# Optimization experiments

Hardware: AMD Instinct MI355X
Metric: run time of the kernel (lower is better)

## Reference

```python
import jax, jax.numpy as jnp
import numpy as np

N_NODES = 50000
N_EDGES = 800000
FEAT = 128
HID = 128
NUM_GRAPHS = 64
ODE_STEPS = 8   # fixed-step RK4 stand-in for adaptive odeint over CFG.ode_time_points
DEPTH = 1.0
EPS = 1e-5


def layer_norm(x, g, b):
    m = jnp.mean(x, axis=-1, keepdims=True)
    v = jnp.var(x, axis=-1, keepdims=True)
    return (x - m) * jax.lax.rsqrt(v + EPS) * g + b


def setup_inputs() -> dict:
    key = jax.random.key(0)
    ks = jax.random.split(key, 16)
    s = 1.0 / np.sqrt(FEAT)
    sh = 1.0 / np.sqrt(HID)
    inp = {
        "x": jax.random.normal(ks[0], (N_NODES, FEAT), jnp.float32),
        "edge_index": jax.random.randint(ks[1], (2, N_EDGES), 0, N_NODES, jnp.int64),
        "batch": jnp.sort(jax.random.randint(ks[2], (N_NODES,), 0, NUM_GRAPHS, jnp.int64)),
        "alpha": jnp.float32(0.8),
        "beta": jnp.float32(0.6),
        "phase": jnp.float32(0.7),
        "W_in": jax.random.normal(ks[3], (FEAT, HID), jnp.float32) * s,
        "b_in": jnp.zeros((HID,), jnp.float32),
        "g_in": jnp.ones((HID,), jnp.float32),
        "be_in": jnp.zeros((HID,), jnp.float32),
        "W_alt": jax.random.normal(ks[4], (FEAT, HID), jnp.float32) * s,
        "b_alt": jnp.zeros((HID,), jnp.float32),
        "g_alt": jnp.ones((HID,), jnp.float32),
        "be_alt": jnp.zeros((HID,), jnp.float32),
        "W_self": jax.random.normal(ks[5], (HID, HID), jnp.float32) * sh,
        "W_msg": jax.random.normal(ks[6], (HID, HID), jnp.float32) * sh,
        "b_ode": jnp.zeros((HID,), jnp.float32),
        "W_int": jax.random.normal(ks[7], (2 * HID, HID), jnp.float32) * sh / np.sqrt(2.0),
        "b_int": jnp.zeros((HID,), jnp.float32),
        "g_int": jnp.ones((HID,), jnp.float32),
        "be_int": jnp.zeros((HID,), jnp.float32),
        "W_out": jax.random.normal(ks[8], (HID, HID), jnp.float32) * sh,
        "b_out": jnp.zeros((HID,), jnp.float32),
    }
    return inp


def _forward(x, alpha, beta, phase,
             W_in, b_in, g_in, be_in,
             W_alt, b_alt, g_alt, be_alt,
             W_self, W_msg, b_ode,
             W_int, b_int, g_int, be_int,
             W_out, b_out,
             edge_index, batch):
    src, dst = edge_index[0], edge_index[1]
    # in-degree for mean aggregation (clamped to 1)
    deg = jax.ops.segment_sum(jnp.ones((src.shape[0],), jnp.float32), dst,
                              num_segments=N_NODES)
    deg = jnp.maximum(deg, 1.0)[:, None]

    # quantum amplitudes -> measurement probabilities (normalized)
    norm = jnp.sqrt(alpha ** 2 + beta ** 2)
    a, b = alpha / norm, beta / norm
    p0, p1 = a ** 2, b ** 2

    # two projection pathways in superposition
    h0 = jax.nn.gelu(layer_norm(x @ W_in + b_in, g_in, be_in))
    h1 = jax.nn.gelu(layer_norm(x @ W_alt + b_alt, g_alt, be_alt))
    h = jnp.sqrt(p0) * h0 + jnp.sqrt(p1) * h1  # [N, H]

    # Neural ODE: dh/dt = tanh(h W_self + mean_{j->i}(h_j W_msg) + b)
    def ode_f(h):
        msg = h[src] @ W_msg                       # [E, H] gather + GEMM
        agg = jax.ops.segment_sum(msg, dst, num_segments=N_NODES) / deg
        return jnp.tanh(h @ W_self + agg + b_ode)

    dt = jnp.float32(DEPTH / ODE_STEPS)

    def rk4_step(h, _):
        k1 = ode_f(h)
        k2 = ode_f(h + 0.5 * dt * k1)
        k3 = ode_f(h + 0.5 * dt * k2)
        k4 = ode_f(h + dt * k3)
        return h + (dt / 6.0) * (k1 + 2.0 * k2 + 2.0 * k3 + k4), None

    h, _ = jax.lax.scan(rk4_step, h, None, length=ODE_STEPS)

    # quantum interference mixing (conditional branch -> masked add)
    interf = 2.0 * jnp.sqrt(p0 * p1) * jnp.cos(phase)
    h_int = jnp.tanh(layer_norm(jnp.concatenate([h, h], axis=-1) @ W_int + b_int,
                                g_int, be_int))
    gate = jnp.where(jnp.abs(interf) > 0.01, interf, 0.0)
    h = h + gate * h_int

    # eval-mode collapse: if p1 >= p0, scale by Re(e^{i*phase}) = cos(phase)
    h = jnp.where(p0 > p1, h, h * jnp.cos(phase))

    h_out = h @ W_out + b_out

    # global mean pool over graphs
    cnt = jax.ops.segment_sum(jnp.ones((N_NODES,), jnp.float32), batch,
                              num_segments=NUM_GRAPHS)
    pooled = jax.ops.segment_sum(h_out, batch, num_segments=NUM_GRAPHS)
    return pooled / jnp.maximum(cnt, 1.0)[:, None]  # [NUM_GRAPHS, H]


def reference(x, edge_index, batch, alpha, beta, phase,
              W_in, b_in, g_in, be_in,
              W_alt, b_alt, g_alt, be_alt,
              W_self, W_msg, b_ode,
              W_int, b_int, g_int, be_int,
              W_out, b_out):
    return _forward(x, alpha, beta, phase,
                    W_in, b_in, g_in, be_in,
                    W_alt, b_alt, g_alt, be_alt,
                    W_self, W_msg, b_ode,
                    W_int, b_int, g_int, be_int,
                    W_out, b_out, edge_index, batch)
```

## Files before the change

### kernel.cpp

```cpp
#include <hip/hip_runtime.h>
#include <math.h>

#define NND 50000
#define NED 800000
#define HD  128
#define NG  64
#define MT  64

typedef __attribute__((ext_vector_type(8))) short short8v;
typedef __attribute__((ext_vector_type(4))) float float4v;
typedef __attribute__((ext_vector_type(2))) float float2v;

__device__ __forceinline__ float gelu_t(float x) {
  const float c = 0.7978845608028654f;
  float t = tanhf(c * (x + 0.044715f * x * x * x));
  return 0.5f * x * (1.0f + t);
}

__device__ __forceinline__ unsigned short f2bf(float f) {
  unsigned int u = __float_as_uint(f);
  u += 0x7FFFu + ((u >> 16) & 1u);
  return (unsigned short)(u >> 16);
}
__device__ __forceinline__ float bf2f(unsigned short s) {
  return __uint_as_float(((unsigned int)s) << 16);
}
__device__ __forceinline__ float bflo(unsigned int u) { return __uint_as_float(u << 16); }
__device__ __forceinline__ float bfhi(unsigned int u) { return __uint_as_float(u & 0xFFFF0000u); }
__device__ __forceinline__ unsigned char f2fp8(float f) {
  return (unsigned char)(__builtin_amdgcn_cvt_pk_fp8_f32(f, f, 0, false) & 0xFF);
}

__global__ void k_hist(const int* __restrict__ dst, int* __restrict__ degi) {
  int e = blockIdx.x * 256 + threadIdx.x;
  if (e < NED) atomicAdd(&degi[dst[e]], 1);
}

__global__ __launch_bounds__(1024) void k_scan(
    const int* __restrict__ degi, int* __restrict__ rowptr,
    int* __restrict__ cursor, float* __restrict__ deginv) {
  __shared__ int wsum[16];
  int tid = threadIdx.x;
  int lane = tid & 63;
  int wid = tid >> 6;
  int running = 0;
  for (int base = 0; base < NND; base += 1024) {
    int idx = base + tid;
    int v = (idx < NND) ? degi[idx] : 0;
    int s = v;
#pragma unroll
    for (int o = 1; o < 64; o <<= 1) {
      int t = __shfl_up(s, o, 64);
      if (lane >= o) s += t;
    }
    if (lane == 63) wsum[wid] = s;
    __syncthreads();
    if (wid == 0) {
      int ws = (lane < 16) ? wsum[lane] : 0;
#pragma unroll
      for (int o = 1; o < 16; o <<= 1) {
        int t = __shfl_up(ws, o, 64);
        if (lane >= o) ws += t;
      }
      if (lane < 16) wsum[lane] = ws;
    }
    __syncthreads();
    int woff = wid ? wsum[wid - 1] : 0;
    int excl = running + woff + s - v;
    if (idx < NND) {
      rowptr[idx] = excl;
      cursor[idx] = excl;
      deginv[idx] = 1.0f / (float)max(v, 1);
    }
    int tot = wsum[15];
    __syncthreads();
    running += tot;
  }
  if (tid == 0) rowptr[NND] = running;
}

__global__ void k_scatter(const int* __restrict__ src, const int* __restrict__ dst,
                          int* __restrict__ cursor, int* __restrict__ csrsrc) {
  int e = blockIdx.x * 256 + threadIdx.x;
  if (e < NED) {
    int d = dst[e];
    int pos = atomicAdd(&cursor[d], 1);
    csrsrc[pos] = src[e];
  }
}

__global__ void k_cnt(const int* __restrict__ batch, float* __restrict__ cnt) {
  int g = threadIdx.x;
  if (g >= NG) return;
  int lo, hi, ub_g, ub_gm1;
  lo = 0; hi = NND;
  while (lo < hi) { int mid = (lo + hi) >> 1; if (batch[mid] <= g) lo = mid + 1; else hi = mid; }
  ub_g = lo;
  if (g == 0) ub_gm1 = 0;
  else {
    lo = 0; hi = NND;
    int v = g - 1;
    while (lo < hi) { int mid = (lo + hi) >> 1; if (batch[mid] <= v) lo = mid + 1; else hi = mid; }
    ub_gm1 = lo;
  }
  cnt[g] = (float)(ub_g - ub_gm1);
}

__global__ void k_weff(const float* __restrict__ Wint, float* __restrict__ weff) {
  int i = blockIdx.x * 256 + threadIdx.x;
  if (i < HD * HD) weff[i] = Wint[i] + Wint[i + HD * HD];
}

__global__ void k_prepB(const float* __restrict__ Wself, const float* __restrict__ Wmsg,
                        unsigned short* __restrict__ Bt) {
  int i = blockIdx.x * 256 + threadIdx.x;
  if (i < 128 * 256) {
    int n = i >> 8, k = i & 255;
    float w = (k < HD) ? Wself[k * HD + n] : Wmsg[(k - HD) * HD + n];
    Bt[i] = f2bf(w);
  }
}

__global__ void k_prepIn(const float* __restrict__ Win, const float* __restrict__ Walt,
                         unsigned short* __restrict__ BtIn) {
  int i = blockIdx.x * 256 + threadIdx.x;
  if (i < 2 * 128 * 128) {
    int p = i >> 14; int rem = i & 16383; int n = rem >> 7; int k = rem & 127;
    const float* W = p ? Walt : Win;
    BtIn[i] = f2bf(W[k * 128 + n]);
  }
}

__global__ __launch_bounds__(256) void k_init2(
    const float* __restrict__ x, const unsigned short* __restrict__ BtIn,
    const float* __restrict__ bin, const float* __restrict__ gin, const float* __restrict__ bein,
    const float* __restrict__ balt, const float* __restrict__ galt, const float* __restrict__ bealt,
    const float* __restrict__ alphap, const float* __restrict__ betap,
    float* __restrict__ hdst, unsigned short* __restrict__ hbf)
{
  __shared__ float red[4][16][2];
  __shared__ unsigned short gtile[2][16][64];
  int tid = threadIdx.x;
  int wave = tid >> 6;
  int lane = tid & 63;
  int l15 = lane & 15;
  int lhi = lane >> 4;
  int path = wave >> 1;
  int colBase = (wave & 1) * 64;
  int rowBase = blockIdx.x * 64;

  const unsigned short* Bp = BtIn + path * 128 * 128;
  short8v bfr[4][4];
#pragma unroll
  for (int t = 0; t < 4; ++t) {
    int n = colBase + t * 16 + l15;
#pragma unroll
    for (int s = 0; s < 4; ++s)
      bfr[t][s] = *(const short8v*)&Bp[n * 128 + s * 32 + lhi * 8];
  }

  const float* bvp = path ? balt : bin;
  const float* gp  = path ? galt : gin;
  const float* bep = path ? bealt : bein;
  float bv[4], gw[4], bew[4];
#pragma unroll
  for (int t = 0; t < 4; ++t) {
    int col = colBase + t * 16 + l15;
    bv[t] = bvp[col]; gw[t] = gp[col]; bew[t] = bep[col];
  }

  float al = alphap[0], btv = betap[0];
  float nrm = sqrtf(al * al + btv * btv);
  float w0 = fabsf(al) / nrm, w1 = fabsf(btv) / nrm;

  for (int rt = 0; rt < 4; ++rt) {
    int arow = rowBase + rt * 16 + l15; if (arow >= NND) arow = NND - 1;
    short8v afr[4];
#pragma unroll
    for (int s = 0; s < 4; ++s) {
      float4 xa = *(const float4*)&x[(size_t)arow * HD + s * 32 + lhi * 8];
      float4 xb = *(const float4*)&x[(size_t)arow * HD + s * 32 + lhi * 8 + 4];
      short8v f;
      f[0] = (short)f2bf(xa.x); f[1] = (short)f2bf(xa.y);
      f[2] = (short)f2bf(xa.z); f[3] = (short)f2bf(xa.w);
      f[4] = (short)f2bf(xb.x); f[5] = (short)f2bf(xb.y);
      f[6] = (short)f2bf(xb.z); f[7] = (short)f2bf(xb.w);
      afr[s] = f;
    }

    float4v acc[4];
#pragma unroll
    for (int t = 0; t < 4; ++t) acc[t] = (float4v){0.f, 0.f, 0.f, 0.f};
#pragma unroll
    for (int s = 0; s < 4; ++s) {
#pragma unroll
      for (int t = 0; t < 4; ++t)
        acc[t] = __builtin_amdgcn_mfma_f32_16x16x32_bf16(afr[s], bfr[t][s], acc[t], 0, 0, 0);
    }

    float z[4][4];
    float psum[4], psq[4];
#pragma unroll
    for (int r = 0; r < 4; ++r) {
      float s1 = 0.f, s2 = 0.f;
#pragma unroll
      for (int t = 0; t < 4; ++t) {
        float zz = acc[t][r] + bv[t];
        z[r][t] = zz;
        s1 += zz; s2 += zz * zz;
      }
#pragma unroll
      for (int m = 1; m < 16; m <<= 1) {
        s1 += __shfl_xor(s1, m, 16);
        s2 += __shfl_xor(s2, m, 16);
      }
      psum[r] = s1; psq[r] = s2;
    }
    if (l15 == 0) {
#pragma unroll
      for (int r = 0; r < 4; ++r) {
        red[wave][lhi * 4 + r][0] = psum[r];
        red[wave][lhi * 4 + r][1] = psq[r];
      }
    }
    __syncthreads();

    int pw = wave ^ 1;
    float gval[4][4];
#pragma unroll
    for (int r = 0; r < 4; ++r) {
      int rowl = lhi * 4 + r;
      float S = psum[r] + red[pw][rowl][0];
      float Q = psq[r]  + red[pw][rowl][1];
      float mean = S * (1.0f / 128.0f);
      float var  = Q * (1.0f / 128.0f) - mean * mean;
      float rs = rsqrtf(var + 1e-5f);
#pragma unroll
      for (int t = 0; t < 4; ++t)
        gval[r][t] = gelu_t((z[r][t] - mean) * rs * gw[t] + bew[t]);
    }

    if (path == 1) {
#pragma unroll
      for (int r = 0; r < 4; ++r)
#pragma unroll
        for (int t = 0; t < 4; ++t)
          gtile[wave & 1][lhi * 4 + r][t * 16 + l15] = f2bf(gval[r][t]);
    }
    __syncthreads();

    if (path == 0) {
#pragma unroll
      for (int r = 0; r < 4; ++r) {
        int m = rowBase + rt * 16 + lhi * 4 + r;
        if (m < NND) {
#pragma unroll
          for (int t = 0; t < 4; ++t) {
            float g1 = bf2f(gtile[wave & 1][lhi * 4 + r][t * 16 + l15]);
            float hv = w0 * gval[r][t] + w1 * g1;
            size_t off = (size_t)m * HD + colBase + t * 16 + l15;
            hdst[off] = hv;
            hbf[off] = f2bf(hv);
          }
        }
      }
    }
    __syncthreads();
  }
}

__global__ __launch_bounds__(256) void k_fused(
    const unsigned short* __restrict__ ain,
    const unsigned short* __restrict__ hbf,
    const unsigned char* __restrict__ k8r,
    unsigned char* __restrict__ k8w,
    unsigned short* __restrict__ usav,
    const int* __restrict__ rowptr, const int* __restrict__ csrsrc,
    const float* __restrict__ deginv,
    const unsigned short* __restrict__ Bt, const float* __restrict__ bode,
    const float* __restrict__ h, float* __restrict__ hacc,
    float* __restrict__ hout, unsigned short* __restrict__ ybf,
    unsigned short* __restrict__ hbfout, int stage)
{
  __shared__ unsigned char u_lds[MT * 256];
  int tid = threadIdx.x;
  int wave = tid >> 6;
  int lane = tid & 63;
  int l15 = lane & 15;
  int lhi = lane >> 4;
  int rowBase = blockIdx.x * MT;
  int ncol0 = wave * 32;

  const float DT = 0.125f;
  float wk = (stage == 0 || stage == 3) ? DT / 6.0f : DT / 3.0f;
  float cy = (stage <= 1) ? 0.5f * DT : DT;
  float cu = (stage == 3) ? DT : 0.5f * DT;

  if (stage == 0) {
    int l16 = tid & 15;
    int grp = tid >> 4;
#pragma unroll
    for (int g = 0; g < MT / 16; ++g) {
      int nloc = g * 16 + grp;
      int node = rowBase + nloc;
      if (node < NND) {
        int e0 = rowptr[node], e1 = rowptr[node + 1];
        float a0=0,a1=0,a2=0,a3=0,a4=0,a5=0,a6=0,a7=0;
        for (int eb = e0; eb < e1; eb += 8) {
          int n8 = e1 - eb; if (n8 > 8) n8 = 8;
          int sidx[8];
#pragma unroll
          for (int j = 0; j < 8; ++j) sidx[j] = csrsrc[eb + ((j < n8) ? j : 0)];
#pragma unroll
          for (int j = 0; j < 8; ++j) {
            if (j < n8) {
              uint4 v = *(const uint4*)&hbf[(size_t)sidx[j] * HD + l16 * 8];
              a0 += bflo(v.x); a1 += bfhi(v.x); a2 += bflo(v.y); a3 += bfhi(v.y);
              a4 += bflo(v.z); a5 += bfhi(v.z); a6 += bflo(v.w); a7 += bfhi(v.w);
            }
          }
        }
        float di = deginv[node];
        uint4 o;
        o.x = (unsigned int)f2bf(a0*di) | ((unsigned int)f2bf(a1*di) << 16);
        o.y = (unsigned int)f2bf(a2*di) | ((unsigned int)f2bf(a3*di) << 16);
        o.z = (unsigned int)f2bf(a4*di) | ((unsigned int)f2bf(a5*di) << 16);
        o.w = (unsigned int)f2bf(a6*di) | ((unsigned int)f2bf(a7*di) << 16);
        unsigned int boff = (unsigned int)nloc * 256u +
            (((unsigned int)l16 * 16u) ^ (((unsigned int)nloc & 7u) << 4));
        *(uint4*)&u_lds[boff] = o;
        *(uint4*)&usav[(size_t)node * HD + l16 * 8] = o;
      }
    }
  } else {
    int l8 = tid & 7;
    int grp = tid >> 3;
#pragma unroll
    for (int g = 0; g < MT / 32; ++g) {
      int nloc = g * 32 + grp;
      int node = rowBase + nloc;
      if (node < NND) {
        int e0 = rowptr[node], e1 = rowptr[node + 1];
        float a[16];
#pragma unroll
        for (int q = 0; q < 16; ++q) a[q] = 0.f;
        for (int eb = e0; eb < e1; eb += 8) {
          int n8 = e1 - eb; if (n8 > 8) n8 = 8;
          int sidx[8];
#pragma unroll
          for (int j = 0; j < 8; ++j) sidx[j] = csrsrc[eb + ((j < n8) ? j : 0)];
#pragma unroll
          for (int j = 0; j < 8; ++j) {
            if (j < n8) {
              uint4 v = *(const uint4*)&k8r[(size_t)sidx[j] * HD + l8 * 16];
              float2v f0 = __builtin_amdgcn_cvt_pk_f32_fp8(v.x, false);
              float2v f1 = __builtin_amdgcn_cvt_pk_f32_fp8(v.x, true);
              float2v f2 = __builtin_amdgcn_cvt_pk_f32_fp8(v.y, false);
              float2v f3 = __builtin_amdgcn_cvt_pk_f32_fp8(v.y, true);
              float2v f4 = __builtin_amdgcn_cvt_pk_f32_fp8(v.z, false);
              float2v f5 = __builtin_amdgcn_cvt_pk_f32_fp8(v.z, true);
              float2v f6 = __builtin_amdgcn_cvt_pk_f32_fp8(v.w, false);
              float2v f7 = __builtin_amdgcn_cvt_pk_f32_fp8(v.w, true);
              a[0]+=f0[0]; a[1]+=f0[1]; a[2]+=f1[0]; a[3]+=f1[1];
              a[4]+=f2[0]; a[5]+=f2[1]; a[6]+=f3[0]; a[7]+=f3[1];
              a[8]+=f4[0]; a[9]+=f4[1]; a[10]+=f5[0]; a[11]+=f5[1];
              a[12]+=f6[0]; a[13]+=f6[1]; a[14]+=f7[0]; a[15]+=f7[1];
            }
          }
        }
        float di = deginv[node] * cu;
        uint4 us0 = *(const uint4*)&usav[(size_t)node * HD + l8 * 16];
        uint4 us1 = *(const uint4*)&usav[(size_t)node * HD + l8 * 16 + 8];
        float u0  = bflo(us0.x) + a[0]*di,  u1  = bfhi(us0.x) + a[1]*di;
        float u2  = bflo(us0.y) + a[2]*di,  u3  = bfhi(us0.y) + a[3]*di;
        float u4  = bflo(us0.z) + a[4]*di,  u5  = bfhi(us0.z) + a[5]*di;
        float u6  = bflo(us0.w) + a[6]*di,  u7  = bfhi(us0.w) + a[7]*di;
        float u8  = bflo(us1.x) + a[8]*di,  u9  = bfhi(us1.x) + a[9]*di;
        float u10 = bflo(us1.y) + a[10]*di, u11 = bfhi(us1.y) + a[11]*di;
        float u12 = bflo(us1.z) + a[12]*di, u13 = bfhi(us1.z) + a[13]*di;
        float u14 = bflo(us1.w) + a[14]*di, u15 = bfhi(us1.w) + a[15]*di;
        uint4 o0, o1;
        o0.x = (unsigned int)f2bf(u0)  | ((unsigned int)f2bf(u1)  << 16);
        o0.y = (unsigned int)f2bf(u2)  | ((unsigned int)f2bf(u3)  << 16);
        o0.z = (unsigned int)f2bf(u4)  | ((unsigned int)f2bf(u5)  << 16);
        o0.w = (unsigned int)f2bf(u6)  | ((unsigned int)f2bf(u7)  << 16);
        o1.x = (unsigned int)f2bf(u8)  | ((unsigned int)f2bf(u9)  << 16);
        o1.y = (unsigned int)f2bf(u10) | ((unsigned int)f2bf(u11) << 16);
        o1.z = (unsigned int)f2bf(u12) | ((unsigned int)f2bf(u13) << 16);
        o1.w = (unsigned int)f2bf(u14) | ((unsigned int)f2bf(u15) << 16);
        unsigned int base = (unsigned int)nloc * 256u;
        unsigned int sw = ((unsigned int)nloc & 7u) << 4;
        *(uint4*)&u_lds[base + (((unsigned int)l8 * 32u) ^ sw)] = o0;
        *(uint4*)&u_lds[base + (((unsigned int)l8 * 32u + 16u) ^ sw)] = o1;
      }
    }
  }

  short8v bfr[2][8];
#pragma unroll
  for (int t = 0; t < 2; ++t) {
    int n = ncol0 + t * 16 + l15;
#pragma unroll
    for (int s = 0; s < 8; ++s) {
      bfr[t][s] = *(const short8v*)&Bt[n * 256 + s * 32 + lhi * 8];
    }
  }
  float bo0 = bode[ncol0 + l15];
  float bo1 = bode[ncol0 + 16 + l15];

  __syncthreads();

#pragma unroll
  for (int rt = 0; rt < MT / 16; ++rt) {
    int rloc = rt * 16 + l15;
    int mload = rowBase + rloc;
    if (mload >= NND) mload = NND - 1;
    short8v afr[8];
#pragma unroll
    for (int s = 0; s < 4; ++s)
      afr[s] = *(const short8v*)&ain[(size_t)mload * HD + s * 32 + lhi * 8];
#pragma unroll
    for (int s = 0; s < 4; ++s) {
      unsigned int boff = (unsigned int)rloc * 256u +
        ((((unsigned int)s * 64u) + ((unsigned int)lhi * 16u)) ^ (((unsigned int)rloc & 7u) << 4));
      afr[4 + s] = *(const short8v*)&u_lds[boff];
    }

    float4v acc0 = {0.f, 0.f, 0.f, 0.f};
    float4v acc1 = {0.f, 0.f, 0.f, 0.f};
#pragma unroll
    for (int s = 0; s < 8; ++s) {
      acc0 = __builtin_amdgcn_mfma_f32_16x16x32_bf16(afr[s], bfr[0][s], acc0, 0, 0, 0);
      acc1 = __builtin_amdgcn_mfma_f32_16x16x32_bf16(afr[s], bfr[1][s], acc1, 0, 0, 0);
    }

#pragma unroll
    for (int t = 0; t < 2; ++t) {
      int n = ncol0 + t * 16 + l15;
      float bo = t ? bo1 : bo0;
#pragma unroll
      for (int r = 0; r < 4; ++r) {
        int m = rowBase + rt * 16 + lhi * 4 + r;
        if (m < NND) {
          size_t off = (size_t)m * HD + n;
          float av = t ? acc1[r] : acc0[r];
          float kv = tanhf(av + bo);
          if (stage == 0) {
            float hv = h[off];
            hacc[off] = hv + wk * kv;
            ybf[off] = f2bf(hv + cy * kv);
            k8w[off] = f2fp8(kv);
          } else if (stage < 3) {
            hacc[off] += wk * kv;
            ybf[off] = f2bf(bf2f(hbf[off]) + cy * kv);
            k8w[off] = f2fp8(kv);
          } else {
            float hn = hacc[off] + wk * kv;
            hout[off] = hn;
            hbfout[off] = f2bf(hn);
          }
        }
      }
    }
  }
}

__global__ __launch_bounds__(256) void k_interf(
    const float* __restrict__ h, const float* __restrict__ weff,
    const float* __restrict__ bint, const float* __restrict__ gint,
    const float* __restrict__ beint,
    const float* __restrict__ alphap, const float* __restrict__ betap,
    const float* __restrict__ phasep,
    float* __restrict__ h2out)
{
  __shared__ float As[64][16];
  __shared__ float Bs[16][128];
  int tid = threadIdx.x;
  int tx = tid & 31, ty = tid >> 5;
  int rowBase = blockIdx.x * 64;
  float acc[8][4];
#pragma unroll
  for (int i = 0; i < 8; ++i) { acc[i][0]=0.f; acc[i][1]=0.f; acc[i][2]=0.f; acc[i][3]=0.f; }

  for (int kc = 0; kc < 8; ++kc) {
    int k0 = kc * 16;
    {
      int r = tid >> 2, kq = (tid & 3) * 4;
      int row = rowBase + r; if (row >= NND) row = NND - 1;
      *(float4*)&As[r][kq] = *(const float4*)&h[(size_t)row * HD + k0 + kq];
    }
#pragma unroll
    for (int j = 0; j < 2; ++j) {
      int kk = (tid >> 5) + j * 8;
      int n = (tid & 31) * 4;
      *(float4*)&Bs[kk][n] = *(const float4*)&weff[(k0 + kk) * HD + n];
    }
    __syncthreads();
#pragma unroll
    for (int kq = 0; kq < 4; ++kq) {
      float4 b0 = *(float4*)&Bs[kq*4+0][tx*4];
      float4 b1 = *(float4*)&Bs[kq*4+1][tx*4];
      float4 b2 = *(float4*)&Bs[kq*4+2][tx*4];
      float4 b3 = *(float4*)&Bs[kq*4+3][tx*4];
#pragma unroll
      for (int i = 0; i < 8; ++i) {
        float4 a = *(float4*)&As[ty*8+i][kq*4];
        acc[i][0] = fmaf(a.x,b0.x,fmaf(a.y,b1.x,fmaf(a.z,b2.x,fmaf(a.w,b3.x,acc[i][0]))));
        acc[i][1] = fmaf(a.x,b0.y,fmaf(a.y,b1.y,fmaf(a.z,b2.y,fmaf(a.w,b3.y,acc[i][1]))));
        acc[i][2] = fmaf(a.x,b0.z,fmaf(a.y,b1.z,fmaf(a.z,b2.z,fmaf(a.w,b3.z,acc[i][2]))));
        acc[i][3] = fmaf(a.x,b0.w,fmaf(a.y,b1.w,fmaf(a.z,b2.w,fmaf(a.w,b3.w,acc[i][3]))));
      }
    }
    __syncthreads();
  }

  float al = alphap[0], bt = betap[0], ph = phasep[0];
  float n2 = al*al + bt*bt;
  float p0 = (al*al) / n2, p1 = (bt*bt) / n2;
  float interf = 2.0f * sqrtf(p0 * p1) * cosf(ph);
  float gate = (fabsf(interf) > 0.01f) ? interf : 0.0f;
  float cscale = (p0 > p1) ? 1.0f : cosf(ph);

  int c0 = tx * 4;
  float4 bi  = *(const float4*)&bint[c0];
  float4 gv  = *(const float4*)&gint[c0];
  float4 bev = *(const float4*)&beint[c0];
#pragma unroll
  for (int i = 0; i < 8; ++i) {
    int row = rowBase + ty*8 + i;
    float z0 = acc[i][0]+bi.x, z1 = acc[i][1]+bi.y, z2 = acc[i][2]+bi.z, z3 = acc[i][3]+bi.w;
    float rsum = z0+z1+z2+z3;
    float rsq  = z0*z0+z1*z1+z2*z2+z3*z3;
#pragma unroll
    for (int m = 1; m < 32; m <<= 1) { rsum += __shfl_xor(rsum, m, 32); rsq += __shfl_xor(rsq, m, 32); }
    float mean = rsum * (1.0f/128.0f);
    float var  = rsq * (1.0f/128.0f) - mean*mean;
    float rs = rsqrtf(var + 1e-5f);
    float t0 = tanhf((z0-mean)*rs*gv.x + bev.x);
    float t1 = tanhf((z1-mean)*rs*gv.y + bev.y);
    float t2 = tanhf((z2-mean)*rs*gv.z + bev.z);
    float t3 = tanhf((z3-mean)*rs*gv.w + bev.w);
    if (row < NND) {
      size_t off = (size_t)row * HD + c0;
      float4 hv = *(const float4*)&h[off];
      float4 o = make_float4((hv.x + gate*t0) * cscale,
                             (hv.y + gate*t1) * cscale,
                             (hv.z + gate*t2) * cscale,
                             (hv.w + gate*t3) * cscale);
      *(float4*)&h2out[off] = o;
    }
  }
}

__global__ __launch_bounds__(256) void k_out(
    const float* __restrict__ h2, const float* __restrict__ Wout,
    const float* __restrict__ bout, const int* __restrict__ batch,
    float* __restrict__ pooled)
{
  __shared__ float As[64][16];
  __shared__ float Bs[16][128];
  int tid = threadIdx.x;
  int tx = tid & 31, ty = tid >> 5;
  int rowBase = blockIdx.x * 64;
  float acc[8][4];
#pragma unroll
  for (int i = 0; i < 8; ++i) { acc[i][0]=0.f; acc[i][1]=0.f; acc[i][2]=0.f; acc[i][3]=0.f; }

  for (int kc = 0; kc < 8; ++kc) {
    int k0 = kc * 16;
    {
      int r = tid >> 2, kq = (tid & 3) * 4;
      int row = rowBase + r; if (row >= NND) row = NND - 1;
      *(float4*)&As[r][kq] = *(const float4*)&h2[(size_t)row * HD + k0 + kq];
    }
#pragma unroll
    for (int j = 0; j < 2; ++j) {
      int kk = (tid >> 5) + j * 8;
      int n = (tid & 31) * 4;
      *(float4*)&Bs[kk][n] = *(const float4*)&Wout[(k0 + kk) * HD + n];
    }
    __syncthreads();
#pragma unroll
    for (int kq = 0; kq < 4; ++kq) {
      float4 b0 = *(float4*)&Bs[kq*4+0][tx*4];
      float4 b1 = *(float4*)&Bs[kq*4+1][tx*4];
      float4 b2 = *(float4*)&Bs[kq*4+2][tx*4];
      float4 b3 = *(float4*)&Bs[kq*4+3][tx*4];
#pragma unroll
      for (int i = 0; i < 8; ++i) {
        float4 a = *(float4*)&As[ty*8+i][kq*4];
        acc[i][0] = fmaf(a.x,b0.x,fmaf(a.y,b1.x,fmaf(a.z,b2.x,fmaf(a.w,b3.x,acc[i][0]))));
        acc[i][1] = fmaf(a.x,b0.y,fmaf(a.y,b1.y,fmaf(a.z,b2.y,fmaf(a.w,b3.y,acc[i][1]))));
        acc[i][2] = fmaf(a.x,b0.z,fmaf(a.y,b1.z,fmaf(a.z,b2.z,fmaf(a.w,b3.z,acc[i][2]))));
        acc[i][3] = fmaf(a.x,b0.w,fmaf(a.y,b1.w,fmaf(a.z,b2.w,fmaf(a.w,b3.w,acc[i][3]))));
      }
    }
    __syncthreads();
  }

  int c0 = tx * 4;
  float4 bo = *(const float4*)&bout[c0];
  int prevg = -1;
  float r0 = 0.f, r1 = 0.f, r2 = 0.f, r3 = 0.f;
#pragma unroll
  for (int i = 0; i < 8; ++i) {
    int row = rowBase + ty*8 + i;
    if (row >= NND) break;
    int g = batch[row];
    float v0 = acc[i][0] + bo.x;
    float v1 = acc[i][1] + bo.y;
    float v2 = acc[i][2] + bo.z;
    float v3 = acc[i][3] + bo.w;
    if (g != prevg) {
      if (prevg >= 0) {
        atomicAdd(&pooled[prevg*HD + c0 + 0], r0);
        atomicAdd(&pooled[prevg*HD + c0 + 1], r1);
        atomicAdd(&pooled[prevg*HD + c0 + 2], r2);
        atomicAdd(&pooled[prevg*HD + c0 + 3], r3);
      }
      prevg = g; r0 = v0; r1 = v1; r2 = v2; r3 = v3;
    } else {
      r0 += v0; r1 += v1; r2 += v2; r3 += v3;
    }
  }
  if (prevg >= 0) {
    atomicAdd(&pooled[prevg*HD + c0 + 0], r0);
    atomicAdd(&pooled[prevg*HD + c0 + 1], r1);
    atomicAdd(&pooled[prevg*HD + c0 + 2], r2);
    atomicAdd(&pooled[prevg*HD + c0 + 3], r3);
  }
}

__global__ void k_final(const float* __restrict__ pooled, const float* __restrict__ cnt,
                        float* __restrict__ out) {
  int i = blockIdx.x * 256 + threadIdx.x;
  if (i < NG * HD) out[i] = pooled[i] / fmaxf(cnt[i >> 7], 1.0f);
}

extern "C" void kernel_launch(void* const* d_in, const int* in_sizes, int n_in,
                              void* d_out, int out_size, void* d_ws, size_t ws_size,
                              hipStream_t stream) {
  (void)in_sizes; (void)n_in; (void)out_size; (void)ws_size;
  const float* x     = (const float*)d_in[0];
  const int*   ei    = (const int*)d_in[1];
  const int*   batch = (const int*)d_in[2];
  const float* alpha = (const float*)d_in[3];
  const float* beta  = (const float*)d_in[4];
  const float* phase = (const float*)d_in[5];
  const float* Win   = (const float*)d_in[6];
  const float* bin   = (const float*)d_in[7];
  const float* gin   = (const float*)d_in[8];
  const float* bein  = (const float*)d_in[9];
  const float* Walt  = (const float*)d_in[10];
  const float* balt  = (const float*)d_in[11];
  const float* galt  = (const float*)d_in[12];
  const float* bealt = (const float*)d_in[13];
  const float* Wself = (const float*)d_in[14];
  const float* Wmsg  = (const float*)d_in[15];
  const float* bode  = (const float*)d_in[16];
  const float* Wint  = (const float*)d_in[17];
  const float* bint  = (const float*)d_in[18];
  const float* gint  = (const float*)d_in[19];
  const float* beint = (const float*)d_in[20];
  const float* Wout  = (const float*)d_in[21];
  const float* bout  = (const float*)d_in[22];
  float* out = (float*)d_out;

  const int* esrc = ei;
  const int* edst = ei + NED;

  size_t NH = (size_t)NND * HD;
  float* h      = (float*)d_ws;
  float* hacc   = h + NH;
  float* deginv = hacc + NH;
  float* weff   = deginv + NND;
  float* pooled = weff + HD * HD;
  float* cnt    = pooled + NG * HD;
  unsigned short* hbf  = (unsigned short*)(cnt + NG);
  unsigned short* ybf  = hbf + NH;
  unsigned short* usav = ybf + NH;
  unsigned short* Bt   = usav + NH;
  unsigned short* BtIn = Bt + 128 * 256;
  unsigned char* k8a = (unsigned char*)(BtIn + 2 * 128 * 128);
  unsigned char* k8b = k8a + NH;
  int* degi   = (int*)(k8b + NH);
  int* rowptr = degi + NND;
  int* cursor = rowptr + (NND + 4);
  int* csrsrc = cursor + NND;

  hipMemsetAsync(degi, 0, NND * sizeof(int), stream);
  hipMemsetAsync(pooled, 0, NG * HD * sizeof(float), stream);

  k_hist   <<<(NED + 255) / 256, 256, 0, stream>>>(edst, degi);
  k_scan   <<<1, 1024, 0, stream>>>(degi, rowptr, cursor, deginv);
  k_scatter<<<(NED + 255) / 256, 256, 0, stream>>>(esrc, edst, cursor, csrsrc);
  k_cnt    <<<1, 64, 0, stream>>>(batch, cnt);
  k_weff   <<<(HD * HD + 255) / 256, 256, 0, stream>>>(Wint, weff);
  k_prepB  <<<128, 256, 0, stream>>>(Wself, Wmsg, Bt);
  k_prepIn <<<128, 256, 0, stream>>>(Win, Walt, BtIn);
  k_init2  <<<(NND + 63) / 64, 256, 0, stream>>>(x, BtIn, bin, gin, bein,
                                                 balt, galt, bealt,
                                                 alpha, beta, h, hbf);
  int nblk = (NND + MT - 1) / MT;
  for (int step = 0; step < 8; ++step) {
    for (int stage = 0; stage < 4; ++stage) {
      const unsigned short* ain = (stage == 0) ? hbf : ybf;
      const unsigned char* k8r = (stage == 2) ? k8b : k8a;
      unsigned char* k8w = (stage == 1) ? k8b : k8a;
      k_fused<<<nblk, 256, 0, stream>>>(ain, hbf, k8r, k8w, usav,
                                        rowptr, csrsrc, deginv, Bt, bode,
                                        h, hacc, h, ybf, hbf, stage);
    }
  }
  k_interf<<<(NND + 63) / 64, 256, 0, stream>>>(h, weff, bint, gint, beint,
                                                alpha, beta, phase, hacc);
  k_out   <<<(NND + 63) / 64, 256, 0, stream>>>(hacc, Wout, bout, batch, pooled);
  k_final <<<(NG * HD + 255) / 256, 256, 0, stream>>>(pooled, cnt, out);
}
```

Before: 2.178 ms.

## Replace fp32 RK4 accumulator with bf16 stage-sum buffer and halve row tile

The fused ODE stage kernel no longer keeps an fp32 running state accumulator. Instead it accumulates the weighted RK4 slopes in a bf16 buffer, reads the bf16 copy of h in stage 0, and folds the sum into the fp32 h only in the last stage. This cuts per-stage global read/write traffic for the state. The row tile shrinks from 64 to 32, which doubles the block count for better load spread. The trade-off is extra rounding error from summing the slopes in bf16.

```diff
diff --git a/kernel.cpp b/kernel.cpp
--- a/kernel.cpp
+++ b/kernel.cpp
@@ -5,7 +5,7 @@
 #define NED 800000
 #define HD  128
 #define NG  64
-#define MT  64
+#define MT  32
 
 typedef __attribute__((ext_vector_type(8))) short short8v;
 typedef __attribute__((ext_vector_type(4))) float float4v;
@@ -275,11 +275,12 @@
     const unsigned char* __restrict__ k8r,
     unsigned char* __restrict__ k8w,
     unsigned short* __restrict__ usav,
+    unsigned short* __restrict__ kacc,
     const int* __restrict__ rowptr, const int* __restrict__ csrsrc,
     const float* __restrict__ deginv,
     const unsigned short* __restrict__ Bt, const float* __restrict__ bode,
-    const float* __restrict__ h, float* __restrict__ hacc,
-    float* __restrict__ hout, unsigned short* __restrict__ ybf,
+    float* __restrict__ hfp,
+    unsigned short* __restrict__ ybf,
     unsigned short* __restrict__ hbfout, int stage)
 {
   __shared__ unsigned char u_lds[MT * 256];
@@ -446,17 +447,16 @@
           float av = t ? acc1[r] : acc0[r];
           float kv = tanhf(av + bo);
           if (stage == 0) {
-            float hv = h[off];
-            hacc[off] = hv + wk * kv;
-            ybf[off] = f2bf(hv + cy * kv);
+            ybf[off] = f2bf(bf2f(hbf[off]) + cy * kv);
+            kacc[off] = f2bf(wk * kv);
             k8w[off] = f2fp8(kv);
           } else if (stage < 3) {
-            hacc[off] += wk * kv;
             ybf[off] = f2bf(bf2f(hbf[off]) + cy * kv);
+            kacc[off] = f2bf(bf2f(kacc[off]) + wk * kv);
             k8w[off] = f2fp8(kv);
           } else {
-            float hn = hacc[off] + wk * kv;
-            hout[off] = hn;
+            float hn = hfp[off] + bf2f(kacc[off]) + wk * kv;
+            hfp[off] = hn;
             hbfout[off] = f2bf(hn);
           }
         }
@@ -671,15 +671,16 @@
 
   size_t NH = (size_t)NND * HD;
   float* h      = (float*)d_ws;
-  float* hacc   = h + NH;
-  float* deginv = hacc + NH;
+  float* h2     = h + NH;
+  float* deginv = h2 + NH;
   float* weff   = deginv + NND;
   float* pooled = weff + HD * HD;
   float* cnt    = pooled + NG * HD;
   unsigned short* hbf  = (unsigned short*)(cnt + NG);
   unsigned short* ybf  = hbf + NH;
   unsigned short* usav = ybf + NH;
-  unsigned short* Bt   = usav + NH;
+  unsigned short* kacc = usav + NH;
+  unsigned short* Bt   = kacc + NH;
   unsigned short* BtIn = Bt + 128 * 256;
   unsigned char* k8a = (unsigned char*)(BtIn + 2 * 128 * 128);
   unsigned char* k8b = k8a + NH;
@@ -707,13 +708,13 @@
       const unsigned short* ain = (stage == 0) ? hbf : ybf;
       const unsigned char* k8r = (stage == 2) ? k8b : k8a;
       unsigned char* k8w = (stage == 1) ? k8b : k8a;
-      k_fused<<<nblk, 256, 0, stream>>>(ain, hbf, k8r, k8w, usav,
+      k_fused<<<nblk, 256, 0, stream>>>(ain, hbf, k8r, k8w, usav, kacc,
                                         rowptr, csrsrc, deginv, Bt, bode,
-                                        h, hacc, h, ybf, hbf, stage);
+                                        h, ybf, hbf, stage);
     }
   }
   k_interf<<<(NND + 63) / 64, 256, 0, stream>>>(h, weff, bint, gint, beint,
-                                                alpha, beta, phase, hacc);
-  k_out   <<<(NND + 63) / 64, 256, 0, stream>>>(hacc, Wout, bout, batch, pooled);
+                                                alpha, beta, phase, h2);
+  k_out   <<<(NND + 63) / 64, 256, 0, stream>>>(h2, Wout, bout, batch, pooled);
   k_final <<<(NG * HD + 255) / 256, 256, 0, stream>>>(pooled, cnt, out);
 }
```

Measured after the change: 2.332 ms. +7.1%, slower.
